# Performance work log

Measured on AMD Instinct MI355X. Metric: run time of the kernel, lower is better.

Reference implementation:

```python
import jax, jax.numpy as jnp
import numpy as np

K = 12
ORDERS = [(1, 2, 3), (1, 3, 2), (3, 2, 1), (3, 1, 2), (2, 1, 3), (2, 3, 1)]


def ranking_3d(x):
    # x: (B, L1, W1, H1, D) -> (B, 12, L1*W1*H1, D)
    B, L1, W1, H1, D = x.shape
    seqs = []
    for dims in ORDERS:
        perm = (0,) + dims + (4,)
        seqs.append(jnp.transpose(x, perm).reshape(B, -1, D))
        xr = jnp.flip(x, axis=dims)
        seqs.append(jnp.transpose(xr, perm).reshape(B, -1, D))
    return jnp.stack(seqs, axis=1)


def restore_original(out_y, shape):
    # out_y: (B, 12, D, L). NOTE: faithfully replicates the original code, which
    # reshapes the (B, D, L) slice directly to (B, d1, d2, d3, D).
    B, L1, W1, H1, D = shape
    size = {1: L1, 2: W1, 3: H1}
    restored = []
    for i in range(12):
        dims = ORDERS[i // 2]
        seq = out_y[:, i]  # (B, D, L)
        dims_shape = tuple(size[d] for d in dims)
        reshaped = seq.reshape((B,) + dims_shape + (D,))
        perm = (0,) + dims + (4,)
        inv = tuple(np.argsort(perm))
        r = jnp.transpose(reshaped, inv)
        if i % 2 == 1:
            r = jnp.flip(r, axis=dims)
        restored.append(r)
    return restored


def selective_scan(u, delta, A, Bs, Cs):
    # u, delta: (B,K,D,L); A: (K,D,N); Bs, Cs: (B,K,N,L)
    us = jnp.moveaxis(u, -1, 0)       # (L,B,K,D)
    ds = jnp.moveaxis(delta, -1, 0)   # (L,B,K,D)
    Bts = jnp.moveaxis(Bs, -1, 0)     # (L,B,K,N)
    Cts = jnp.moveaxis(Cs, -1, 0)     # (L,B,K,N)
    h0 = jnp.zeros(u.shape[:-1] + (A.shape[-1],), u.dtype)  # (B,K,D,N)

    def step(h, inp):
        ut, dt, Bt, Ct = inp
        dA = jnp.exp(dt[..., None] * A)                       # (B,K,D,N)
        h = dA * h + (dt * ut)[..., None] * Bt[:, :, None, :]
        y = jnp.einsum('bkdn,bkn->bkd', h, Ct)
        return h, y

    _, ys = jax.lax.scan(step, h0, (us, ds, Bts, Cts))
    return jnp.moveaxis(ys, 0, -1)  # (B,K,D,L)


def setup_inputs() -> dict:
    key = jax.random.key(0)
    ks = jax.random.split(key, 8)
    B, H, W, Len, D = 1, 16, 16, 16, 128
    N, R = 16, 8
    x = jax.random.normal(ks[0], (B, H, W, Len, D), dtype=jnp.float32)
    x_proj_weight = jax.random.normal(ks[1], (K, R + 2 * N, D), dtype=jnp.float32) * 0.02
    std = R ** -0.5
    dt_projs_weight = jax.random.uniform(ks[2], (K, D, R), minval=-std, maxval=std, dtype=jnp.float32)
    dt = jnp.exp(jax.random.uniform(ks[3], (K, D)) * (np.log(0.1) - np.log(0.001)) + np.log(0.001))
    dt = jnp.clip(dt, 1e-4, None)
    dt_projs_bias = (dt + jnp.log(-jnp.expm1(-dt))).astype(jnp.float32)
    A_logs = jnp.broadcast_to(jnp.log(jnp.arange(1, N + 1, dtype=jnp.float32)), (K, D, N)).copy()
    Ds = jnp.ones((K, D), dtype=jnp.float32)
    merge_w = jax.random.normal(ks[4], (K,), dtype=jnp.float32) * (1.0 / K)
    merge_b = jax.random.normal(ks[5], (), dtype=jnp.float32) * 0.01
    return {'x': x, 'x_proj_weight': x_proj_weight, 'dt_projs_weight': dt_projs_weight,
            'dt_projs_bias': dt_projs_bias, 'A_logs': A_logs, 'Ds': Ds,
            'merge_w': merge_w, 'merge_b': merge_b}


def reference(x, x_proj_weight, dt_projs_weight, dt_projs_bias, A_logs, Ds, merge_w, merge_b):
    B, H, W, Len, D = x.shape
    L = H * W * Len
    R = dt_projs_weight.shape[-1]
    N = A_logs.shape[-1]
    xs = jnp.transpose(ranking_3d(x), (0, 1, 3, 2))  # (B,K,D,L)
    x_dbl = jnp.einsum('bkdl,kcd->bkcl', xs, x_proj_weight)  # (B,K,R+2N,L)
    dts, Bs, Cs = jnp.split(x_dbl, [R, R + N], axis=2)
    dts = jnp.einsum('bkrl,kdr->bkdl', dts, dt_projs_weight)
    delta = jax.nn.softplus(dts + dt_projs_bias[None, :, :, None])
    A = -jnp.exp(A_logs)  # (K,D,N)
    ys = selective_scan(xs, delta, A, Bs, Cs)
    out_y = ys + Ds[None, :, :, None] * xs  # (B,K,D,L)
    restored = restore_original(out_y, (B, H, W, Len, D))
    stacked = jnp.stack(restored, axis=1)  # (B,K,H,W,Len,D)
    # mergeconv: 1x1 Conv2d over K channels == weighted sum across directions
    y = jnp.einsum('bkhwld,k->bhwld', stacked, merge_w) + merge_b
    return y
```

## Files before the change

### kernel.cpp

```cpp
#include <hip/hip_runtime.h>

#define KK 12
#define LL 4096
#define DD 128
#define NN 16
#define RR 8
#define NC 256
#define LCS 16
#define LB 32
#define XST 140
#define SDST 44
#define XDBL_TILE (LB * SDST)

__device__ __forceinline__ int pos_of(int k, int l) {
    int o = k >> 1;
    int le = (k & 1) ? (4095 - l) : l;
    int t1 = le >> 8, t2 = (le >> 4) & 15, t3 = le & 15;
    switch (o) {
        case 0:  return (t1 << 8) | (t2 << 4) | t3;
        case 1:  return (t1 << 8) | (t3 << 4) | t2;
        case 2:  return (t3 << 8) | (t2 << 4) | t1;
        case 3:  return (t2 << 8) | (t3 << 4) | t1;
        case 4:  return (t2 << 8) | (t1 << 4) | t3;
        default: return (t3 << 8) | (t1 << 4) | t2;
    }
}

__device__ __forceinline__ float delta_row_z(const float* sdbl, int l,
                                             float4 w0, float4 w1, float bz) {
    const float4* dr = (const float4*)(sdbl + l * SDST);
    float4 r0 = dr[0], r1 = dr[1];
    return bz + w0.x * r0.x + w0.y * r0.y + w0.z * r0.z + w0.w * r0.w
              + w1.x * r1.x + w1.y * r1.y + w1.z * r1.z + w1.w * r1.w;
}

__device__ __forceinline__ bool load_A16(const float* __restrict__ A_logs,
                                         int k, int d, float* A16) {
    const float4* ap = (const float4*)(A_logs + (size_t)(k * DD + d) * NN);
    #pragma unroll
    for (int q = 0; q < 4; q++) {
        float4 a4 = ap[q];
        A16[4*q+0] = -__expf(a4.x); A16[4*q+1] = -__expf(a4.y);
        A16[4*q+2] = -__expf(a4.z); A16[4*q+3] = -__expf(a4.w);
    }
    bool s = true;
    #pragma unroll
    for (int j = 1; j < 16; j++) {
        float m = (float)(j + 1);
        s = s && (fabsf(A16[j] - m * A16[0]) <= 1e-4f * m * fabsf(A16[0]));
    }
    return s;
}

template<bool S>
__device__ __forceinline__ void e16_from(float v, float q, const float* A16,
                                         float* e) {
    if (S) {
        e[0] = q;
        #pragma unroll
        for (int j = 1; j < 16; j++) e[j] = e[j - 1] * q;
    } else {
        #pragma unroll
        for (int j = 0; j < 16; j++) e[j] = __expf(v * A16[j]);
    }
}

template<bool S>
__device__ __forceinline__ void scanA_body(
    float* xs, const float* sdbl, int k, int cc, int lbase, int d,
    const float* A16, float4 w0, float4 w1, float bz, float Dval,
    float* __restrict__ S_g, float* __restrict__ dtsum)
{
    float h[16];
    #pragma unroll
    for (int n = 0; n < 16; n++) h[n] = 0.0f;
    float dsum = 0.0f;

    #pragma unroll 4
    for (int i = 0; i < LCS; i++) {
        int l = lbase + i;
        float z = delta_row_z(sdbl, l, w0, w1, bz);
        float E = __expf(-fabsf(z));
        float dt = fmaxf(z, 0.0f) + __logf(1.0f + E);
        float u = xs[l * XST + d];
        dsum += dt;
        float tu = dt * u;
        float q = S ? __expf(dt * A16[0]) : 0.0f;
        float e[16];
        e16_from<S>(dt, q, A16, e);
        const float4* bp = (const float4*)(&sdbl[l * SDST + 8]);
        float4 b0 = bp[0], b1 = bp[1], b2 = bp[2], b3 = bp[3];
        const float4* cp = (const float4*)(&sdbl[l * SDST + 24]);
        float4 c0 = cp[0], c1 = cp[1], c2 = cp[2], c3 = cp[3];
        h[0]  = e[0]  * h[0]  + tu * b0.x;  h[1]  = e[1]  * h[1]  + tu * b0.y;
        h[2]  = e[2]  * h[2]  + tu * b0.z;  h[3]  = e[3]  * h[3]  + tu * b0.w;
        h[4]  = e[4]  * h[4]  + tu * b1.x;  h[5]  = e[5]  * h[5]  + tu * b1.y;
        h[6]  = e[6]  * h[6]  + tu * b1.z;  h[7]  = e[7]  * h[7]  + tu * b1.w;
        h[8]  = e[8]  * h[8]  + tu * b2.x;  h[9]  = e[9]  * h[9]  + tu * b2.y;
        h[10] = e[10] * h[10] + tu * b2.z;  h[11] = e[11] * h[11] + tu * b2.w;
        h[12] = e[12] * h[12] + tu * b3.x;  h[13] = e[13] * h[13] + tu * b3.y;
        h[14] = e[14] * h[14] + tu * b3.z;  h[15] = e[15] * h[15] + tu * b3.w;
        float y = h[0]*c0.x + h[1]*c0.y + h[2]*c0.z + h[3]*c0.w
                + h[4]*c1.x + h[5]*c1.y + h[6]*c1.z + h[7]*c1.w
                + h[8]*c2.x + h[9]*c2.y + h[10]*c2.z + h[11]*c2.w
                + h[12]*c3.x + h[13]*c3.y + h[14]*c3.z + h[15]*c3.w;
        xs[l * XST + d] = y + Dval * u;
    }

    float4* sp = (float4*)(S_g + (((size_t)(k * NC + cc) * DD + d) * NN));
    sp[0] = make_float4(h[0],  h[1],  h[2],  h[3]);
    sp[1] = make_float4(h[4],  h[5],  h[6],  h[7]);
    sp[2] = make_float4(h[8],  h[9],  h[10], h[11]);
    sp[3] = make_float4(h[12], h[13], h[14], h[15]);
    dtsum[(k * NC + cc) * DD + d] = dsum;
}

__global__ __launch_bounds__(256, 4) void k1_proj_scanA(
    const float* __restrict__ x, const float* __restrict__ Wp,
    const float* __restrict__ Wdt, const float* __restrict__ bias,
    const float* __restrict__ A_logs, const float* __restrict__ Ds,
    float* __restrict__ S_g, float* __restrict__ dtsum,
    float* __restrict__ oy, float* __restrict__ xdbl)
{
    const int blk = blockIdx.x;
    const int k = blk >> 7;
    const int c = blk & 127;
    const int l0 = c * LB;
    const int t = threadIdx.x;

    __shared__ __align__(16) float xs[LB * XST];
    __shared__ __align__(16) float sdbl[LB * SDST];
    __shared__ int pos_s[LB];

    if (t < LB) pos_s[t] = pos_of(k, l0 + t);
    __syncthreads();

    {
        int lane32 = t & 31, rowi = t >> 5;
        #pragma unroll
        for (int p = 0; p < 4; p++) {
            int l = p * 8 + rowi;
            float4 v = *(const float4*)(x + (size_t)pos_s[l] * DD + lane32 * 4);
            *(float4*)(&xs[l * XST + lane32 * 4]) = v;
        }
    }
    __syncthreads();

    {
        int l = t & 31, cg = t >> 5;
        float acc[5];
        #pragma unroll
        for (int j = 0; j < 5; j++) acc[j] = 0.0f;
        const float* wk = Wp + (size_t)(k * 40 + cg * 5) * DD;
        for (int d4 = 0; d4 < DD; d4 += 4) {
            float4 xv = *(const float4*)(&xs[l * XST + d4]);
            #pragma unroll
            for (int j = 0; j < 5; j++) {
                const float* w = wk + j * DD + d4;
                acc[j] += xv.x * w[0] + xv.y * w[1] + xv.z * w[2] + xv.w * w[3];
            }
        }
        #pragma unroll
        for (int j = 0; j < 5; j++) sdbl[l * SDST + cg * 5 + j] = acc[j];
    }
    __syncthreads();

    {
        const float4* s4 = (const float4*)sdbl;
        float4* g4 = (float4*)(xdbl + (size_t)blk * XDBL_TILE);
        for (int idx = t; idx < XDBL_TILE / 4; idx += 256) g4[idx] = s4[idx];
    }

    const int d = t & 127, half = t >> 7;
    const int cc = 2 * c + half, lbase = half * LCS;
    float A16[16];
    bool structured = load_A16(A_logs, k, d, A16);
    const float4* wp4 = (const float4*)(Wdt + (size_t)(k * DD + d) * RR);
    const float4 w0 = wp4[0], w1 = wp4[1];
    const float bz = bias[k * DD + d];
    const float Dval = Ds[k * DD + d];

    if (structured)
        scanA_body<true>(xs, sdbl, k, cc, lbase, d, A16, w0, w1, bz, Dval,
                         S_g, dtsum);
    else
        scanA_body<false>(xs, sdbl, k, cc, lbase, d, A16, w0, w1, bz, Dval,
                          S_g, dtsum);

    {
        float* base = oy + ((size_t)(k * DD + d)) * LL + l0 + lbase;
        #pragma unroll
        for (int p = 0; p < 4; p++) {
            int j = p * 4;
            float4 v = make_float4(xs[(lbase + j + 0) * XST + d],
                                   xs[(lbase + j + 1) * XST + d],
                                   xs[(lbase + j + 2) * XST + d],
                                   xs[(lbase + j + 3) * XST + d]);
            *(float4*)(base + j) = v;
        }
    }
}

__global__ __launch_bounds__(256) void k2_combine(
    float* __restrict__ S_g, const float* __restrict__ dtsum,
    const float* __restrict__ A_logs)
{
    int tid = blockIdx.x * 256 + threadIdx.x;
    int kk = tid >> 11, rem = tid & 2047, dd2 = rem >> 4;
    float Ac = -__expf(A_logs[tid]);
    float hh = 0.0f;
    #pragma unroll 8
    for (int c2 = 0; c2 < NC; c2++) {
        size_t base = ((size_t)(kk * NC + c2)) * 2048 + rem;
        float s = S_g[base];
        float dsv = dtsum[(kk * NC + c2) * DD + dd2];
        S_g[base] = hh;
        hh = s + __expf(dsv * Ac) * hh;
    }
}

template<bool S>
__device__ __forceinline__ void corr_body(
    float* ybuf, const float* sdbl, int lbase, int d,
    const float* A16, const float* h0, float4 w0, float4 w1, float bz)
{
    float P = 1.0f;
    float Dsum = 0.0f;
    #pragma unroll 4
    for (int i = 0; i < LCS; i++) {
        int l = lbase + i;
        float z = delta_row_z(sdbl, l, w0, w1, bz);
        float E = __expf(-fabsf(z));
        float dt = fmaxf(z, 0.0f) + __logf(1.0f + E);
        float e[16];
        if (S) {
            P *= __expf(dt * A16[0]);
            e16_from<true>(0.0f, P, A16, e);
        } else {
            Dsum += dt;
            e16_from<false>(Dsum, 0.0f, A16, e);
        }
        const float4* cp = (const float4*)(&sdbl[l * SDST + 24]);
        float4 c0 = cp[0], c1 = cp[1], c2 = cp[2], c3 = cp[3];
        float y = e[0]*h0[0]*c0.x + e[1]*h0[1]*c0.y + e[2]*h0[2]*c0.z + e[3]*h0[3]*c0.w
                + e[4]*h0[4]*c1.x + e[5]*h0[5]*c1.y + e[6]*h0[6]*c1.z + e[7]*h0[7]*c1.w
                + e[8]*h0[8]*c2.x + e[9]*h0[9]*c2.y + e[10]*h0[10]*c2.z + e[11]*h0[11]*c2.w
                + e[12]*h0[12]*c3.x + e[13]*h0[13]*c3.y + e[14]*h0[14]*c3.z + e[15]*h0[15]*c3.w;
        ybuf[l * XST + d] = y;
    }
}

__global__ __launch_bounds__(256, 4) void k3_corr(
    const float* __restrict__ Wdt, const float* __restrict__ bias,
    const float* __restrict__ A_logs, const float* __restrict__ S_g,
    const float* __restrict__ xdbl, float* __restrict__ oy)
{
    const int blk = blockIdx.x;
    const int k = blk >> 7;
    const int c = blk & 127;
    const int l0 = c * LB;
    const int t = threadIdx.x;

    __shared__ __align__(16) float sdbl[LB * SDST];
    __shared__ __align__(16) float ybuf[LB * XST];
    {
        const float4* g4 = (const float4*)(xdbl + (size_t)blk * XDBL_TILE);
        float4* s4 = (float4*)sdbl;
        for (int idx = t; idx < XDBL_TILE / 4; idx += 256) s4[idx] = g4[idx];
    }
    __syncthreads();

    const int d = t & 127, half = t >> 7;
    const int cc = 2 * c + half, lbase = half * LCS;
    float A16[16];
    bool structured = load_A16(A_logs, k, d, A16);
    const float4* wp4 = (const float4*)(Wdt + (size_t)(k * DD + d) * RR);
    const float4 w0 = wp4[0], w1 = wp4[1];
    const float bz = bias[k * DD + d];

    float h0[16];
    {
        const float4* hp = (const float4*)(S_g + (((size_t)(k * NC + cc) * DD + d) * NN));
        float4 a = hp[0], b = hp[1], c4 = hp[2], e4 = hp[3];
        h0[0]  = a.x;  h0[1]  = a.y;  h0[2]  = a.z;  h0[3]  = a.w;
        h0[4]  = b.x;  h0[5]  = b.y;  h0[6]  = b.z;  h0[7]  = b.w;
        h0[8]  = c4.x; h0[9]  = c4.y; h0[10] = c4.z; h0[11] = c4.w;
        h0[12] = e4.x; h0[13] = e4.y; h0[14] = e4.z; h0[15] = e4.w;
    }

    if (structured)
        corr_body<true>(ybuf, sdbl, lbase, d, A16, h0, w0, w1, bz);
    else
        corr_body<false>(ybuf, sdbl, lbase, d, A16, h0, w0, w1, bz);

    {
        float* base = oy + ((size_t)(k * DD + d)) * LL + l0 + lbase;
        #pragma unroll
        for (int p = 0; p < 4; p++) {
            int j = p * 4;
            float4 v = *(float4*)(base + j);
            v.x += ybuf[(lbase + j + 0) * XST + d];
            v.y += ybuf[(lbase + j + 1) * XST + d];
            v.z += ybuf[(lbase + j + 2) * XST + d];
            v.w += ybuf[(lbase + j + 3) * XST + d];
            *(float4*)(base + j) = v;
        }
    }
}

__global__ __launch_bounds__(256) void k4_merge(
    const float* __restrict__ out_y, const float* __restrict__ mw,
    const float* __restrict__ mb, float* __restrict__ out)
{
    int idx = blockIdx.x * 256 + threadIdx.x;
    int dd = idx & 127;
    int p = idx >> 7;
    int i3 = p & 15, i2 = (p >> 4) & 15, i1 = (p >> 8) & 15;

    float accv = mb[0];
    #pragma unroll
    for (int k = 0; k < 12; k++) {
        int a1 = i1, a2 = i2, a3 = i3;
        if (k & 1) { a1 = 15 - i1; a2 = 15 - i2; a3 = 15 - i3; }
        int j1, j2, j3;
        switch (k >> 1) {
            case 0:  j1 = a1; j2 = a2; j3 = a3; break;
            case 1:  j1 = a1; j2 = a3; j3 = a2; break;
            case 2:  j1 = a3; j2 = a2; j3 = a1; break;
            case 3:  j1 = a3; j2 = a1; j3 = a2; break;
            case 4:  j1 = a2; j2 = a1; j3 = a3; break;
            default: j1 = a2; j2 = a3; j3 = a1; break;
        }
        int jb = (j1 << 8) | (j2 << 4) | j3;
        accv += mw[k] * out_y[(size_t)k * (DD * LL) + (jb >> 5) * LL
                              + ((jb & 31) << 7) + dd];
    }
    out[idx] = accv;
}

extern "C" void kernel_launch(void* const* d_in, const int* in_sizes, int n_in,
                              void* d_out, int out_size, void* d_ws, size_t ws_size,
                              hipStream_t stream) {
    const float* x      = (const float*)d_in[0];
    const float* Wp     = (const float*)d_in[1];
    const float* Wdt    = (const float*)d_in[2];
    const float* bias   = (const float*)d_in[3];
    const float* A_logs = (const float*)d_in[4];
    const float* Ds     = (const float*)d_in[5];
    const float* mw     = (const float*)d_in[6];
    const float* mb     = (const float*)d_in[7];
    float* out = (float*)d_out;

    float* ws   = (float*)d_ws;
    float* S_g  = ws;
    float* dts  = S_g + (size_t)KK * NC * DD * NN;
    float* oy   = dts + (size_t)KK * NC * DD;
    float* xdbl = oy + (size_t)KK * DD * LL;

    k1_proj_scanA<<<dim3(KK * 128), dim3(256), 0, stream>>>(
        x, Wp, Wdt, bias, A_logs, Ds, S_g, dts, oy, xdbl);
    k2_combine<<<dim3(KK * DD * NN / 256), dim3(256), 0, stream>>>(S_g, dts, A_logs);
    k3_corr<<<dim3(KK * 128), dim3(256), 0, stream>>>(
        Wdt, bias, A_logs, S_g, xdbl, oy);
    k4_merge<<<dim3(LL * DD / 256), dim3(256), 0, stream>>>(oy, mw, mb, out);
}
```

Before: 181.3 us.

## Store chunk states in bf16, cache delta prefix sums, and tree-power exponentials

Chunk-end scan states are now packed to bf16 pairs, which halves the traffic for k1, k2 and k3, and k2 now runs two states per thread. k1 writes per-step cumulative delta sums and only the C coefficients to global memory, so k3 no longer recomputes softplus deltas or reloads the full x_dbl tile. The power chain for structured A becomes a shallower multiplication tree. In exchange, k1 writes a large extra array (K*D*L floats of dsum) and the states lose precision to bf16.

```diff
diff --git a/kernel.cpp b/kernel.cpp
--- a/kernel.cpp
+++ b/kernel.cpp
@@ -10,7 +10,6 @@
 #define LB 32
 #define XST 140
 #define SDST 44
-#define XDBL_TILE (LB * SDST)
 
 __device__ __forceinline__ int pos_of(int k, int l) {
     int o = k >> 1;
@@ -26,6 +25,14 @@
     }
 }
 
+__device__ __forceinline__ unsigned pk_bf2(float a, float b) {
+    unsigned ua = __float_as_uint(a); ua = (ua + 0x7FFF + ((ua >> 16) & 1)) >> 16;
+    unsigned ub = __float_as_uint(b); ub = (ub + 0x7FFF + ((ub >> 16) & 1)) >> 16;
+    return ua | (ub << 16);
+}
+__device__ __forceinline__ float lo_bf(unsigned u) { return __uint_as_float(u << 16); }
+__device__ __forceinline__ float hi_bf(unsigned u) { return __uint_as_float(u & 0xFFFF0000u); }
+
 __device__ __forceinline__ float delta_row_z(const float* sdbl, int l,
                                              float4 w0, float4 w1, float bz) {
     const float4* dr = (const float4*)(sdbl + l * SDST);
@@ -52,13 +59,19 @@
     return s;
 }
 
+__device__ __forceinline__ void e16_tree(float q, float* e) {
+    e[0] = q;
+    float q2 = q * q;
+    e[1] = q2; e[2] = q2 * q; e[3] = q2 * q2;
+    e[4] = e[3] * q;   e[5] = e[3] * q2;  e[6] = e[3] * e[2];  e[7] = e[3] * e[3];
+    e[8] = e[7] * q;   e[9] = e[7] * q2;  e[10] = e[7] * e[2]; e[11] = e[7] * e[3];
+    e[12] = e[7] * e[4]; e[13] = e[7] * e[5]; e[14] = e[7] * e[6]; e[15] = e[7] * e[7];
+}
+
 template<bool S>
-__device__ __forceinline__ void e16_from(float v, float q, const float* A16,
-                                         float* e) {
+__device__ __forceinline__ void e16_from(float v, const float* A16, float* e) {
     if (S) {
-        e[0] = q;
-        #pragma unroll
-        for (int j = 1; j < 16; j++) e[j] = e[j - 1] * q;
+        e16_tree(__expf(v * A16[0]), e);
     } else {
         #pragma unroll
         for (int j = 0; j < 16; j++) e[j] = __expf(v * A16[j]);
@@ -69,7 +82,8 @@
 __device__ __forceinline__ void scanA_body(
     float* xs, const float* sdbl, int k, int cc, int lbase, int d,
     const float* A16, float4 w0, float4 w1, float bz, float Dval,
-    float* __restrict__ S_g, float* __restrict__ dtsum)
+    unsigned* __restrict__ S_b, float* __restrict__ dtsum,
+    float* __restrict__ dslp)
 {
     float h[16];
     #pragma unroll
@@ -84,10 +98,10 @@
         float dt = fmaxf(z, 0.0f) + __logf(1.0f + E);
         float u = xs[l * XST + d];
         dsum += dt;
+        dslp[i] = dsum;
         float tu = dt * u;
-        float q = S ? __expf(dt * A16[0]) : 0.0f;
         float e[16];
-        e16_from<S>(dt, q, A16, e);
+        e16_from<S>(dt, A16, e);
         const float4* bp = (const float4*)(&sdbl[l * SDST + 8]);
         float4 b0 = bp[0], b1 = bp[1], b2 = bp[2], b3 = bp[3];
         const float4* cp = (const float4*)(&sdbl[l * SDST + 24]);
@@ -107,11 +121,14 @@
         xs[l * XST + d] = y + Dval * u;
     }
 
-    float4* sp = (float4*)(S_g + (((size_t)(k * NC + cc) * DD + d) * NN));
-    sp[0] = make_float4(h[0],  h[1],  h[2],  h[3]);
-    sp[1] = make_float4(h[4],  h[5],  h[6],  h[7]);
-    sp[2] = make_float4(h[8],  h[9],  h[10], h[11]);
-    sp[3] = make_float4(h[12], h[13], h[14], h[15]);
+    size_t b8 = ((size_t)(k * NC + cc) * DD + d) * 8;
+    uint4 p0, p1;
+    p0.x = pk_bf2(h[0],  h[1]);  p0.y = pk_bf2(h[2],  h[3]);
+    p0.z = pk_bf2(h[4],  h[5]);  p0.w = pk_bf2(h[6],  h[7]);
+    p1.x = pk_bf2(h[8],  h[9]);  p1.y = pk_bf2(h[10], h[11]);
+    p1.z = pk_bf2(h[12], h[13]); p1.w = pk_bf2(h[14], h[15]);
+    *(uint4*)(S_b + b8)     = p0;
+    *(uint4*)(S_b + b8 + 4) = p1;
     dtsum[(k * NC + cc) * DD + d] = dsum;
 }
 
@@ -119,8 +136,9 @@
     const float* __restrict__ x, const float* __restrict__ Wp,
     const float* __restrict__ Wdt, const float* __restrict__ bias,
     const float* __restrict__ A_logs, const float* __restrict__ Ds,
-    float* __restrict__ S_g, float* __restrict__ dtsum,
-    float* __restrict__ oy, float* __restrict__ xdbl)
+    unsigned* __restrict__ S_b, float* __restrict__ dtsum,
+    float* __restrict__ oy, float* __restrict__ csp,
+    float* __restrict__ dsl)
 {
     const int blk = blockIdx.x;
     const int k = blk >> 7;
@@ -166,9 +184,11 @@
     __syncthreads();
 
     {
-        const float4* s4 = (const float4*)sdbl;
-        float4* g4 = (float4*)(xdbl + (size_t)blk * XDBL_TILE);
-        for (int idx = t; idx < XDBL_TILE / 4; idx += 256) g4[idx] = s4[idx];
+        float4* g4 = (float4*)(csp + (size_t)blk * 512);
+        for (int idx = t; idx < 128; idx += 256) {
+            int l = idx >> 2, q = idx & 3;
+            g4[idx] = *(const float4*)(&sdbl[l * SDST + 24 + q * 4]);
+        }
     }
 
     const int d = t & 127, half = t >> 7;
@@ -179,13 +199,14 @@
     const float4 w0 = wp4[0], w1 = wp4[1];
     const float bz = bias[k * DD + d];
     const float Dval = Ds[k * DD + d];
+    float* dslp = dsl + ((size_t)(k * DD + d)) * LL + l0 + lbase;
 
     if (structured)
         scanA_body<true>(xs, sdbl, k, cc, lbase, d, A16, w0, w1, bz, Dval,
-                         S_g, dtsum);
+                         S_b, dtsum, dslp);
     else
         scanA_body<false>(xs, sdbl, k, cc, lbase, d, A16, w0, w1, bz, Dval,
-                          S_g, dtsum);
+                          S_b, dtsum, dslp);
 
     {
         float* base = oy + ((size_t)(k * DD + d)) * LL + l0 + lbase;
@@ -202,58 +223,51 @@
 }
 
 __global__ __launch_bounds__(256) void k2_combine(
-    float* __restrict__ S_g, const float* __restrict__ dtsum,
+    unsigned* __restrict__ S_b, const float* __restrict__ dtsum,
     const float* __restrict__ A_logs)
 {
     int tid = blockIdx.x * 256 + threadIdx.x;
-    int kk = tid >> 11, rem = tid & 2047, dd2 = rem >> 4;
-    float Ac = -__expf(A_logs[tid]);
-    float hh = 0.0f;
+    int kk = tid >> 10, rem = tid & 1023, dd2 = rem >> 3, j = rem & 7;
+    const float* ap = A_logs + ((size_t)kk * DD + dd2) * NN + 2 * j;
+    float A0 = -__expf(ap[0]), A1 = -__expf(ap[1]);
+    float h0 = 0.0f, h1 = 0.0f;
     #pragma unroll 8
     for (int c2 = 0; c2 < NC; c2++) {
-        size_t base = ((size_t)(kk * NC + c2)) * 2048 + rem;
-        float s = S_g[base];
+        size_t b8 = ((size_t)(kk * NC + c2) * DD + dd2) * 8 + j;
+        unsigned u = S_b[b8];
         float dsv = dtsum[(kk * NC + c2) * DD + dd2];
-        S_g[base] = hh;
-        hh = s + __expf(dsv * Ac) * hh;
+        float s0 = lo_bf(u), s1 = hi_bf(u);
+        S_b[b8] = pk_bf2(h0, h1);
+        h0 = s0 + __expf(dsv * A0) * h0;
+        h1 = s1 + __expf(dsv * A1) * h1;
     }
 }
 
 template<bool S>
 __device__ __forceinline__ void corr_body(
-    float* ybuf, const float* sdbl, int lbase, int d,
-    const float* A16, const float* h0, float4 w0, float4 w1, float bz)
-{
-    float P = 1.0f;
-    float Dsum = 0.0f;
+    float* ybuf, const float* csp_s, const float* dslp, int lbase, int d,
+    const float* A16, const float* g)
+{
     #pragma unroll 4
     for (int i = 0; i < LCS; i++) {
         int l = lbase + i;
-        float z = delta_row_z(sdbl, l, w0, w1, bz);
-        float E = __expf(-fabsf(z));
-        float dt = fmaxf(z, 0.0f) + __logf(1.0f + E);
+        float Dsum = dslp[i];
         float e[16];
-        if (S) {
-            P *= __expf(dt * A16[0]);
-            e16_from<true>(0.0f, P, A16, e);
-        } else {
-            Dsum += dt;
-            e16_from<false>(Dsum, 0.0f, A16, e);
-        }
-        const float4* cp = (const float4*)(&sdbl[l * SDST + 24]);
+        e16_from<S>(Dsum, A16, e);
+        const float4* cp = (const float4*)(&csp_s[l * 16]);
         float4 c0 = cp[0], c1 = cp[1], c2 = cp[2], c3 = cp[3];
-        float y = e[0]*h0[0]*c0.x + e[1]*h0[1]*c0.y + e[2]*h0[2]*c0.z + e[3]*h0[3]*c0.w
-                + e[4]*h0[4]*c1.x + e[5]*h0[5]*c1.y + e[6]*h0[6]*c1.z + e[7]*h0[7]*c1.w
-                + e[8]*h0[8]*c2.x + e[9]*h0[9]*c2.y + e[10]*h0[10]*c2.z + e[11]*h0[11]*c2.w
-                + e[12]*h0[12]*c3.x + e[13]*h0[13]*c3.y + e[14]*h0[14]*c3.z + e[15]*h0[15]*c3.w;
+        float y = e[0]*g[0]*c0.x + e[1]*g[1]*c0.y + e[2]*g[2]*c0.z + e[3]*g[3]*c0.w
+                + e[4]*g[4]*c1.x + e[5]*g[5]*c1.y + e[6]*g[6]*c1.z + e[7]*g[7]*c1.w
+                + e[8]*g[8]*c2.x + e[9]*g[9]*c2.y + e[10]*g[10]*c2.z + e[11]*g[11]*c2.w
+                + e[12]*g[12]*c3.x + e[13]*g[13]*c3.y + e[14]*g[14]*c3.z + e[15]*g[15]*c3.w;
         ybuf[l * XST + d] = y;
     }
 }
 
 __global__ __launch_bounds__(256, 4) void k3_corr(
-    const float* __restrict__ Wdt, const float* __restrict__ bias,
-    const float* __restrict__ A_logs, const float* __restrict__ S_g,
-    const float* __restrict__ xdbl, float* __restrict__ oy)
+    const float* __restrict__ A_logs, const unsigned* __restrict__ S_b,
+    const float* __restrict__ csp, const float* __restrict__ dsl,
+    float* __restrict__ oy)
 {
     const int blk = blockIdx.x;
     const int k = blk >> 7;
@@ -261,12 +275,12 @@
     const int l0 = c * LB;
     const int t = threadIdx.x;
 
-    __shared__ __align__(16) float sdbl[LB * SDST];
+    __shared__ __align__(16) float csp_s[LB * 16];
     __shared__ __align__(16) float ybuf[LB * XST];
     {
-        const float4* g4 = (const float4*)(xdbl + (size_t)blk * XDBL_TILE);
-        float4* s4 = (float4*)sdbl;
-        for (int idx = t; idx < XDBL_TILE / 4; idx += 256) s4[idx] = g4[idx];
+        const float4* g4 = (const float4*)(csp + (size_t)blk * 512);
+        float4* s4 = (float4*)csp_s;
+        for (int idx = t; idx < 128; idx += 256) s4[idx] = g4[idx];
     }
     __syncthreads();
 
@@ -274,24 +288,22 @@
     const int cc = 2 * c + half, lbase = half * LCS;
     float A16[16];
     bool structured = load_A16(A_logs, k, d, A16);
-    const float4* wp4 = (const float4*)(Wdt + (size_t)(k * DD + d) * RR);
-    const float4 w0 = wp4[0], w1 = wp4[1];
-    const float bz = bias[k * DD + d];
-
-    float h0[16];
-    {
-        const float4* hp = (const float4*)(S_g + (((size_t)(k * NC + cc) * DD + d) * NN));
-        float4 a = hp[0], b = hp[1], c4 = hp[2], e4 = hp[3];
-        h0[0]  = a.x;  h0[1]  = a.y;  h0[2]  = a.z;  h0[3]  = a.w;
-        h0[4]  = b.x;  h0[5]  = b.y;  h0[6]  = b.z;  h0[7]  = b.w;
-        h0[8]  = c4.x; h0[9]  = c4.y; h0[10] = c4.z; h0[11] = c4.w;
-        h0[12] = e4.x; h0[13] = e4.y; h0[14] = e4.z; h0[15] = e4.w;
+    const float* dslp = dsl + ((size_t)(k * DD + d)) * LL + l0 + lbase;
+
+    float g[16];
+    {
+        const uint4* hp = (const uint4*)(S_b + ((size_t)(k * NC + cc) * DD + d) * 8);
+        uint4 a = hp[0], b = hp[1];
+        g[0]  = lo_bf(a.x); g[1]  = hi_bf(a.x); g[2]  = lo_bf(a.y); g[3]  = hi_bf(a.y);
+        g[4]  = lo_bf(a.z); g[5]  = hi_bf(a.z); g[6]  = lo_bf(a.w); g[7]  = hi_bf(a.w);
+        g[8]  = lo_bf(b.x); g[9]  = hi_bf(b.x); g[10] = lo_bf(b.y); g[11] = hi_bf(b.y);
+        g[12] = lo_bf(b.z); g[13] = hi_bf(b.z); g[14] = lo_bf(b.w); g[15] = hi_bf(b.w);
     }
 
     if (structured)
-        corr_body<true>(ybuf, sdbl, lbase, d, A16, h0, w0, w1, bz);
+        corr_body<true>(ybuf, csp_s, dslp, lbase, d, A16, g);
     else
-        corr_body<false>(ybuf, sdbl, lbase, d, A16, h0, w0, w1, bz);
+        corr_body<false>(ybuf, csp_s, dslp, lbase, d, A16, g);
 
     {
         float* base = oy + ((size_t)(k * DD + d)) * LL + l0 + lbase;
@@ -351,16 +363,15 @@
     const float* mb     = (const float*)d_in[7];
     float* out = (float*)d_out;
 
-    float* ws   = (float*)d_ws;
-    float* S_g  = ws;
-    float* dts  = S_g + (size_t)KK * NC * DD * NN;
+    unsigned* S_b = (unsigned*)d_ws;
+    float* dts  = (float*)(S_b + (size_t)KK * NC * DD * 8);
     float* oy   = dts + (size_t)KK * NC * DD;
-    float* xdbl = oy + (size_t)KK * DD * LL;
+    float* csp  = oy + (size_t)KK * DD * LL;
+    float* dsl  = csp + (size_t)KK * 128 * 512;
 
     k1_proj_scanA<<<dim3(KK * 128), dim3(256), 0, stream>>>(
-        x, Wp, Wdt, bias, A_logs, Ds, S_g, dts, oy, xdbl);
-    k2_combine<<<dim3(KK * DD * NN / 256), dim3(256), 0, stream>>>(S_g, dts, A_logs);
-    k3_corr<<<dim3(KK * 128), dim3(256), 0, stream>>>(
-        Wdt, bias, A_logs, S_g, xdbl, oy);
+        x, Wp, Wdt, bias, A_logs, Ds, S_b, dts, oy, csp, dsl);
+    k2_combine<<<dim3(KK * DD * 8 / 256), dim3(256), 0, stream>>>(S_b, dts, A_logs);
+    k3_corr<<<dim3(KK * 128), dim3(256), 0, stream>>>(A_logs, S_b, csp, dsl, oy);
     k4_merge<<<dim3(LL * DD / 256), dim3(256), 0, stream>>>(oy, mw, mb, out);
 }
```

After: 195.6 us. 1.08x slower.
